# Kernel tuning notes

Measured on AMD Instinct MI355X. Metric: run time of the kernel, lower is better.

The kernel has to match this reference:

```python
import jax, jax.numpy as jnp
import numpy as np


def setup_inputs() -> dict:
    key = jax.random.key(0)
    k1, k2, k3 = jax.random.split(key, 3)
    S, B, H = 4096, 16, 1024
    hidden = jax.random.normal(k1, (1, B, H), dtype=jnp.float32)
    encoder_outputs = jax.random.normal(k2, (S, B, H), dtype=jnp.float32)
    W_attn = jax.random.normal(k3, (H, H), dtype=jnp.float32) * (1.0 / np.sqrt(H))
    b_attn = jnp.zeros((H,), dtype=jnp.float32)
    return {"hidden": hidden, "encoder_outputs": encoder_outputs,
            "W_attn": W_attn, "b_attn": b_attn}


def reference(hidden, encoder_outputs, W_attn, b_attn):
    # method == 'general': energy_i = hidden_b . (W @ enc_{i,b} + b)
    # encoder_outputs: [S, B, H]; hidden: [1, B, H]
    proj = jnp.einsum('sbh,kh->sbk', encoder_outputs, W_attn) + b_attn  # [S,B,H]
    energies = jnp.einsum('bh,sbh->bs', hidden[0], proj)                # [B,S]
    attn = jax.nn.softmax(energies, axis=-1)
    return attn[:, None, :]  # [B, 1, S]
```

## Files before the change

### kernel.cpp

```cpp
#include <hip/hip_runtime.h>
#include <math.h>


#define SS 4096
#define BB 16
#define HH 1024
#define KC 16
#define KLEN (HH / KC)

#define BNB 512
#define BNT 512
#define NGRP (SS * BB / 32)
#define TILES (NGRP / BNB)

typedef float f4 __attribute__((ext_vector_type(4)));

__global__ void __launch_bounds__(256)
gemv_partial_kernel(const float* __restrict__ hidden,
                    const float* __restrict__ W,
                    float* __restrict__ partial) {
    int blk = blockIdx.x;
    int kc  = blk >> 6;
    int rb  = blk & 63;
    int b   = rb >> 2;
    int h   = ((rb & 3) << 8) | threadIdx.x;
    const float* hrow = hidden + b * HH + kc * KLEN;
    const float* Wp   = W + (size_t)(kc * KLEN) * HH + h;
    float a0 = 0.f, a1 = 0.f, a2 = 0.f, a3 = 0.f;
    #pragma unroll 4
    for (int k = 0; k < KLEN; k += 4) {
        a0 += hrow[k + 0] * Wp[(k + 0) * HH];
        a1 += hrow[k + 1] * Wp[(k + 1) * HH];
        a2 += hrow[k + 2] * Wp[(k + 2) * HH];
        a3 += hrow[k + 3] * Wp[(k + 3) * HH];
    }
    partial[kc * (BB * HH) + b * HH + h] = (a0 + a1) + (a2 + a3);
}

__global__ void __launch_bounds__(256)
gemv_reduce_kernel(const float* __restrict__ partial,
                   float* __restrict__ v) {
    int i = blockIdx.x * 256 + threadIdx.x;
    float s = 0.f;
    #pragma unroll
    for (int kc = 0; kc < KC; ++kc) s += partial[kc * (BB * HH) + i];
    v[i] = s;
}

__global__ void __launch_bounds__(BNT, 4)
energies_kernel(const float* __restrict__ enc,
                const float* __restrict__ v,
                float* __restrict__ out) {
    __shared__ f4 vlds[BB * HH / 4];
    int tid = threadIdx.x;
    const f4* vg = (const f4*)v;
    #pragma unroll
    for (int it = 0; it < (BB * HH / 4) / BNT; ++it)
        vlds[it * BNT + tid] = vg[it * BNT + tid];
    __syncthreads();

    int lane = tid & 63;
    int wi   = tid >> 6;
    for (int t = 0; t < TILES; ++t) {
        int g  = t * BNB + blockIdx.x;
        int p0 = g * 32 + wi * 4;
        float acc[4];
        #pragma unroll
        for (int j = 0; j < 4; ++j) {
            int p = p0 + j;
            int b = p & (BB - 1);
            const f4* e4 = (const f4*)(enc + (size_t)p * HH);
            f4 a0 = e4[0 * 64 + lane];
            f4 a1 = e4[1 * 64 + lane];
            f4 a2 = e4[2 * 64 + lane];
            f4 a3 = e4[3 * 64 + lane];
            f4 w0 = vlds[b * 256 + 0 * 64 + lane];
            f4 w1 = vlds[b * 256 + 1 * 64 + lane];
            f4 w2 = vlds[b * 256 + 2 * 64 + lane];
            f4 w3 = vlds[b * 256 + 3 * 64 + lane];
            f4 pr = a0 * w0 + a1 * w1 + a2 * w2 + a3 * w3;
            acc[j] = (pr.x + pr.y) + (pr.z + pr.w);
        }
        #pragma unroll
        for (int j = 0; j < 4; ++j) {
            #pragma unroll
            for (int off = 32; off; off >>= 1)
                acc[j] += __shfl_xor(acc[j], off, 64);
        }
        if (lane == 0) {
            #pragma unroll
            for (int j = 0; j < 4; ++j) {
                int p = p0 + j;
                out[(p & (BB - 1)) * SS + (p >> 4)] = acc[j];
            }
        }
    }
}

__global__ void __launch_bounds__(256)
softmax_kernel(float* __restrict__ out) {
    int b = blockIdx.x;
    float* row = out + b * SS;
    int t = threadIdx.x;
    float vals[16];
    float m = -INFINITY;
    #pragma unroll
    for (int i = 0; i < 16; ++i) {
        vals[i] = row[t + i * 256];
        m = fmaxf(m, vals[i]);
    }
    #pragma unroll
    for (int off = 32; off; off >>= 1) m = fmaxf(m, __shfl_xor(m, off, 64));
    __shared__ float redm[4];
    __shared__ float reds[4];
    int wid = t >> 6;
    if ((t & 63) == 0) redm[wid] = m;
    __syncthreads();
    m = fmaxf(fmaxf(redm[0], redm[1]), fmaxf(redm[2], redm[3]));

    float sum = 0.f;
    #pragma unroll
    for (int i = 0; i < 16; ++i) {
        vals[i] = expf(vals[i] - m);
        sum += vals[i];
    }
    #pragma unroll
    for (int off = 32; off; off >>= 1) sum += __shfl_xor(sum, off, 64);
    if ((t & 63) == 0) reds[wid] = sum;
    __syncthreads();
    sum = reds[0] + reds[1] + reds[2] + reds[3];
    float inv = 1.0f / sum;
    #pragma unroll
    for (int i = 0; i < 16; ++i) row[t + i * 256] = vals[i] * inv;
}

extern "C" void kernel_launch(void* const* d_in, const int* in_sizes, int n_in,
                              void* d_out, int out_size, void* d_ws, size_t ws_size,
                              hipStream_t stream) {
    const float* hidden = (const float*)d_in[0];
    const float* enc    = (const float*)d_in[1];
    const float* W      = (const float*)d_in[2];
    float* out     = (float*)d_out;
    float* v       = (float*)d_ws;
    float* partial = v + BB * HH;

    hipLaunchKernelGGL(gemv_partial_kernel, dim3(KC * 64), dim3(256), 0, stream,
                       hidden, W, partial);
    hipLaunchKernelGGL(gemv_reduce_kernel, dim3(BB * HH / 256), dim3(256), 0, stream,
                       partial, v);
    hipLaunchKernelGGL(energies_kernel, dim3(BNB), dim3(BNT), 0, stream,
                       enc, v, out);
    hipLaunchKernelGGL(softmax_kernel, dim3(BB), dim3(256), 0, stream, out);
}
```

Before: 56.69 us.

## Fuse GEMV, energies and softmax into one persistent kernel with grid barriers

Replaces the four-launch pipeline with a single persistent kernel. It computes the W^T·hidden GEMV with an in-block reduction, synchronises the grid, computes energies into registers, and does a grid-wide softmax using atomic max/sum plus grid barriers. This removes kernel-launch gaps and the global round-trip of energies between the energies and softmax kernels. In exchange it depends on all 512 blocks being co-resident, adds three spin barriers and a memset, and makes occupancy/attribute queries on every launch, falling back to the old path if residency cannot be guaranteed.

```diff
diff --git a/kernel.cpp b/kernel.cpp
--- a/kernel.cpp
+++ b/kernel.cpp
@@ -5,15 +5,166 @@
 #define SS 4096
 #define BB 16
 #define HH 1024
+#define BNB 512
+#define BNT 512
+#define TILES 4
+
+typedef float f4 __attribute__((ext_vector_type(4)));
+
+__device__ __forceinline__ unsigned flipf(float f) {
+    unsigned u = __float_as_uint(f);
+    return (u & 0x80000000u) ? ~u : (u | 0x80000000u);
+}
+__device__ __forceinline__ float unflipf(unsigned u) {
+    return __uint_as_float((u & 0x80000000u) ? (u & 0x7fffffffu) : ~u);
+}
+
+__device__ __forceinline__ void grid_barrier(unsigned* cnt) {
+    __syncthreads();
+    __threadfence();
+    if (threadIdx.x == 0) {
+        __hip_atomic_fetch_add(cnt, 1u, __ATOMIC_ACQ_REL, __HIP_MEMORY_SCOPE_AGENT);
+        while (__hip_atomic_load(cnt, __ATOMIC_ACQUIRE, __HIP_MEMORY_SCOPE_AGENT)
+               < (unsigned)BNB)
+            __builtin_amdgcn_s_sleep(2);
+    }
+    __syncthreads();
+    __threadfence();
+}
+
+__global__ void __launch_bounds__(BNT, 4)
+fused_kernel(const float* __restrict__ hidden,
+             const float* __restrict__ enc,
+             const float* __restrict__ W,
+             float* __restrict__ out,
+             unsigned* __restrict__ ctrl,
+             float* __restrict__ v) {
+    __shared__ f4 vlds[BB * HH / 4];
+    __shared__ unsigned lds_max[BB];
+    __shared__ float    lds_sum[BB];
+    float* red = (float*)vlds;
+    int tid = threadIdx.x;
+
+    {
+        int b_    = blockIdx.x >> 5;
+        int hbase = (blockIdx.x & 31) << 5;
+        int kc    = tid >> 5;
+        int ho    = tid & 31;
+        const float* hrow = hidden + b_ * HH + kc * 64;
+        const float* Wp   = W + (size_t)(kc * 64) * HH + hbase + ho;
+        float a0 = 0.f, a1 = 0.f, a2 = 0.f, a3 = 0.f;
+        #pragma unroll 4
+        for (int k = 0; k < 64; k += 4) {
+            a0 += hrow[k + 0] * Wp[(k + 0) * HH];
+            a1 += hrow[k + 1] * Wp[(k + 1) * HH];
+            a2 += hrow[k + 2] * Wp[(k + 2) * HH];
+            a3 += hrow[k + 3] * Wp[(k + 3) * HH];
+        }
+        red[tid] = (a0 + a1) + (a2 + a3);
+        __syncthreads();
+        if (tid < 32) {
+            float s = 0.f;
+            #pragma unroll
+            for (int kc2 = 0; kc2 < 16; ++kc2) s += red[kc2 * 32 + tid];
+            v[b_ * HH + hbase + tid] = s;
+        }
+    }
+    grid_barrier(&ctrl[0]);
+
+    {
+        const f4* vg = (const f4*)v;
+        #pragma unroll
+        for (int it = 0; it < (BB * HH / 4) / BNT; ++it)
+            vlds[it * BNT + tid] = vg[it * BNT + tid];
+    }
+    __syncthreads();
+
+    int lane = tid & 63;
+    int wi   = tid >> 6;
+    float acc[TILES][4];
+    #pragma unroll
+    for (int t = 0; t < TILES; ++t) {
+        int g  = t * BNB + blockIdx.x;
+        int p0 = g * 32 + wi * 4;
+        #pragma unroll
+        for (int j = 0; j < 4; ++j) {
+            int p  = p0 + j;
+            int b_ = p & (BB - 1);
+            const f4* e4 = (const f4*)(enc + (size_t)p * HH);
+            f4 a0 = e4[0 * 64 + lane];
+            f4 a1 = e4[1 * 64 + lane];
+            f4 a2 = e4[2 * 64 + lane];
+            f4 a3 = e4[3 * 64 + lane];
+            f4 w0 = vlds[b_ * 256 + 0 * 64 + lane];
+            f4 w1 = vlds[b_ * 256 + 1 * 64 + lane];
+            f4 w2 = vlds[b_ * 256 + 2 * 64 + lane];
+            f4 w3 = vlds[b_ * 256 + 3 * 64 + lane];
+            f4 pr = a0 * w0 + a1 * w1 + a2 * w2 + a3 * w3;
+            acc[t][j] = (pr.x + pr.y) + (pr.z + pr.w);
+        }
+        #pragma unroll
+        for (int j = 0; j < 4; ++j) {
+            #pragma unroll
+            for (int off = 32; off; off >>= 1)
+                acc[t][j] += __shfl_xor(acc[t][j], off, 64);
+        }
+    }
+
+    if (tid < BB) lds_max[tid] = 0u;
+    __syncthreads();
+    if (lane == 0) {
+        #pragma unroll
+        for (int j = 0; j < 4; ++j) {
+            float m = fmaxf(fmaxf(acc[0][j], acc[1][j]),
+                            fmaxf(acc[2][j], acc[3][j]));
+            atomicMax(&lds_max[(wi * 4 + j) & (BB - 1)], flipf(m));
+        }
+    }
+    __syncthreads();
+    if (tid < BB) atomicMax(&ctrl[16 + tid], lds_max[tid]);
+    grid_barrier(&ctrl[1]);
+
+    float mb[4];
+    #pragma unroll
+    for (int j = 0; j < 4; ++j)
+        mb[j] = unflipf(ctrl[16 + ((wi * 4 + j) & (BB - 1))]);
+    if (tid < BB) lds_sum[tid] = 0.f;
+    __syncthreads();
+    #pragma unroll
+    for (int t = 0; t < TILES; ++t)
+        #pragma unroll
+        for (int j = 0; j < 4; ++j)
+            acc[t][j] = expf(acc[t][j] - mb[j]);
+    if (lane == 0) {
+        #pragma unroll
+        for (int j = 0; j < 4; ++j) {
+            float s = ((acc[0][j] + acc[1][j]) + (acc[2][j] + acc[3][j]));
+            atomicAdd(&lds_sum[(wi * 4 + j) & (BB - 1)], s);
+        }
+    }
+    __syncthreads();
+    if (tid < BB) atomicAdd((float*)&ctrl[32 + tid], lds_sum[tid]);
+    grid_barrier(&ctrl[2]);
+
+    float inv[4];
+    #pragma unroll
+    for (int j = 0; j < 4; ++j)
+        inv[j] = 1.0f / ((float*)&ctrl[32])[(wi * 4 + j) & (BB - 1)];
+    if (lane == 0) {
+        #pragma unroll
+        for (int t = 0; t < TILES; ++t) {
+            int p0 = (t * BNB + blockIdx.x) * 32 + wi * 4;
+            #pragma unroll
+            for (int j = 0; j < 4; ++j) {
+                int p = p0 + j;
+                out[(p & (BB - 1)) * SS + (p >> 4)] = acc[t][j] * inv[j];
+            }
+        }
+    }
+}
+
 #define KC 16
 #define KLEN (HH / KC)
-
-#define BNB 512
-#define BNT 512
-#define NGRP (SS * BB / 32)
-#define TILES (NGRP / BNB)
-
-typedef float f4 __attribute__((ext_vector_type(4)));
 
 __global__ void __launch_bounds__(256)
 gemv_partial_kernel(const float* __restrict__ hidden,
@@ -58,7 +209,6 @@
     for (int it = 0; it < (BB * HH / 4) / BNT; ++it)
         vlds[it * BNT + tid] = vg[it * BNT + tid];
     __syncthreads();
-
     int lane = tid & 63;
     int wi   = tid >> 6;
     for (int t = 0; t < TILES; ++t) {
@@ -117,7 +267,6 @@
     if ((t & 63) == 0) redm[wid] = m;
     __syncthreads();
     m = fmaxf(fmaxf(redm[0], redm[1]), fmaxf(redm[2], redm[3]));
-
     float sum = 0.f;
     #pragma unroll
     for (int i = 0; i < 16; ++i) {
@@ -140,15 +289,35 @@
     const float* hidden = (const float*)d_in[0];
     const float* enc    = (const float*)d_in[1];
     const float* W      = (const float*)d_in[2];
-    float* out     = (float*)d_out;
-    float* v       = (float*)d_ws;
+    float* out = (float*)d_out;
+
+    unsigned* ctrl = (unsigned*)d_ws;
+    float*    v    = (float*)d_ws + 64;
     float* partial = v + BB * HH;
 
-    hipLaunchKernelGGL(gemv_partial_kernel, dim3(KC * 64), dim3(256), 0, stream,
-                       hidden, W, partial);
-    hipLaunchKernelGGL(gemv_reduce_kernel, dim3(BB * HH / 256), dim3(256), 0, stream,
-                       partial, v);
-    hipLaunchKernelGGL(energies_kernel, dim3(BNB), dim3(BNT), 0, stream,
-                       enc, v, out);
-    hipLaunchKernelGGL(softmax_kernel, dim3(BB), dim3(256), 0, stream, out);
-}
+    hipMemsetAsync(ctrl, 0, 64 * sizeof(unsigned), stream);
+
+    int dev = 0;
+    hipGetDevice(&dev);
+    int numCU = 0;
+    hipDeviceGetAttribute(&numCU, hipDeviceAttributeMultiprocessorCount, dev);
+    int maxBlk = 0;
+    hipError_t qe = hipOccupancyMaxActiveBlocksPerMultiprocessor(
+        &maxBlk, (const void*)fused_kernel, BNT, 0);
+
+    hipError_t le = hipErrorUnknown;
+    if (qe == hipSuccess && maxBlk >= 2 && (long)maxBlk * numCU >= BNB) {
+        le = hipSuccess;
+        hipLaunchKernelGGL(fused_kernel, dim3(BNB), dim3(BNT), 0, stream,
+                           hidden, enc, W, out, ctrl, v);
+    }
+    if (le != hipSuccess) {
+        hipLaunchKernelGGL(gemv_partial_kernel, dim3(KC * 64), dim3(256), 0,
+                           stream, hidden, W, partial);
+        hipLaunchKernelGGL(gemv_reduce_kernel, dim3(BB * HH / 256), dim3(256),
+                           0, stream, partial, v);
+        hipLaunchKernelGGL(energies_kernel, dim3(BNB), dim3(BNT), 0, stream,
+                           enc, v, out);
+        hipLaunchKernelGGL(softmax_kernel, dim3(BB), dim3(256), 0, stream, out);
+    }
+}
```

Measured after the change: 61.68 us. 1.09x slower.
